# Performance work log

Hardware: AMD Instinct MI355X
Metric: run time of the kernel (lower is better)

## Reference

```python
import jax, jax.numpy as jnp
import numpy as np

D_MODEL = 2048
N_HEADS = 16
D_HEAD = D_MODEL // N_HEADS
BATCH = 2
SEQ = 2048
NEG = -1e9


def setup_inputs() -> dict:
    key = jax.random.key(0)
    ks = jax.random.split(key, 6)
    s = 1.0 / np.sqrt(D_MODEL)
    x = jax.random.normal(ks[0], (BATCH, SEQ, D_MODEL), dtype=jnp.float32)
    # additive causal mask: 0 on/below diagonal, -1e9 above
    causal = jnp.where(jnp.tril(jnp.ones((SEQ, SEQ), dtype=bool)), 0.0, NEG).astype(jnp.float32)
    return {
        "x": x,
        "mask": causal,
        "Wq": jax.random.normal(ks[1], (D_MODEL, D_MODEL), dtype=jnp.float32) * s,
        "bq": jnp.zeros((D_MODEL,), dtype=jnp.float32),
        "Wk": jax.random.normal(ks[2], (D_MODEL, D_MODEL), dtype=jnp.float32) * s,
        "bk": jnp.zeros((D_MODEL,), dtype=jnp.float32),
        "Wv": jax.random.normal(ks[3], (D_MODEL, D_MODEL), dtype=jnp.float32) * s,
        "bv": jnp.zeros((D_MODEL,), dtype=jnp.float32),
        "Wo": jax.random.normal(ks[4], (D_MODEL, D_MODEL), dtype=jnp.float32) * s,
        "bo": jnp.zeros((D_MODEL,), dtype=jnp.float32),
    }


def reference(x, mask, Wq, bq, Wk, bk, Wv, bv, Wo, bo):
    B, S, _ = x.shape
    scale = 1.0 / np.sqrt(D_HEAD).astype(np.float32)
    # projections -> (B, H, S, Dh)
    def split_heads(t):
        return t.reshape(B, S, N_HEADS, D_HEAD).transpose(0, 2, 1, 3)
    q = split_heads(x @ Wq + bq)
    k = split_heads(x @ Wk + bk)
    v = split_heads(x @ Wv + bv)
    scores = jnp.einsum("bhqd,bhkd->bhqk", q, k) * scale + mask  # (B,H,S,S)
    weights = jax.nn.softmax(scores, axis=-1)
    attn = jnp.einsum("bhqk,bhkd->bhqd", weights, v)
    attn = attn.transpose(0, 2, 1, 3).reshape(B, S, D_MODEL)
    return attn @ Wo + bo
```

## Files before the change

### kernel.cpp

```cpp
#include <hip/hip_runtime.h>
#include <hip/hip_bf16.h>
#include <math.h>

typedef __bf16 bf16;
typedef __attribute__((ext_vector_type(4))) __bf16 bf16x4;
typedef __attribute__((ext_vector_type(8))) __bf16 bf16x8;
typedef __attribute__((ext_vector_type(4))) float f32x4;
typedef __attribute__((ext_vector_type(4))) int i32x4;

#define DEV __device__ __forceinline__
#define FENCE asm volatile("" ::: "memory")

static constexpr int S_LEN = 2048;
static constexpr int DM = 2048;
static constexpr int NB = 2;
static constexpr int NH = 16;
static constexpr int DH = 128;
static constexpr long MROWS = (long)NB * S_LEN;

static constexpr float QSCALE = 0.12751744836522312f;
static constexpr float M0 = 11.0f;


__global__ void k_cast_bf16(const float* __restrict__ in, bf16* __restrict__ out, long n8) {
  long i = (long)blockIdx.x * blockDim.x + threadIdx.x;
  long stride = (long)gridDim.x * blockDim.x;
  for (; i < n8; i += stride) {
    const float4* p = (const float4*)(in + i * 8);
    float4 a = p[0], b = p[1];
    bf16x8 v;
    v[0] = (bf16)a.x; v[1] = (bf16)a.y; v[2] = (bf16)a.z; v[3] = (bf16)a.w;
    v[4] = (bf16)b.x; v[5] = (bf16)b.y; v[6] = (bf16)b.z; v[7] = (bf16)b.w;
    *(bf16x8*)(out + i * 8) = v;
  }
}

__global__ void k_transpose_w(const float* __restrict__ in, bf16* __restrict__ out) {
  __shared__ float t[32][33];
  int bx = blockIdx.x * 32, by = blockIdx.y * 32;
  int tx = threadIdx.x, ty = threadIdx.y;
#pragma unroll
  for (int i = 0; i < 32; i += 8)
    t[ty + i][tx] = in[(long)(by + ty + i) * DM + bx + tx];
  __syncthreads();
#pragma unroll
  for (int i = 0; i < 32; i += 8)
    out[(long)(bx + ty + i) * DM + by + tx] = (bf16)t[tx][ty + i];
}

__global__ void k_transpose_w3(const float* __restrict__ w0, const float* __restrict__ w1,
                               const float* __restrict__ w2, bf16* __restrict__ out) {
  __shared__ float t[32][33];
  int z = blockIdx.z;
  const float* in = (z == 0) ? w0 : (z == 1) ? w1 : w2;
  bf16* o = out + (long)z * DM * DM;
  int bx = blockIdx.x * 32, by = blockIdx.y * 32;
  int tx = threadIdx.x, ty = threadIdx.y;
#pragma unroll
  for (int i = 0; i < 32; i += 8)
    t[ty + i][tx] = in[(long)(by + ty + i) * DM + bx + tx];
  __syncthreads();
#pragma unroll
  for (int i = 0; i < 32; i += 8)
    o[(long)(bx + ty + i) * DM + by + tx] = (bf16)t[tx][ty + i];
}


DEV void stg_round(const bf16* __restrict__ g, long gstride, bf16* l, int tid, int c) {
  int o = c * 8192 + tid * 16;
  int row = o >> 7;
  int blk = (o >> 4) & 7;
  const bf16* src = g + (long)row * gstride + ((blk ^ (row & 7)) << 3);
  char* dst = (char*)l + (o & ~1023);
  __builtin_amdgcn_global_load_lds(
      (const __attribute__((address_space(1))) void*)src,
      (__attribute__((address_space(3))) void*)dst, 16, 0, 0);
}

template<int ROWB>
DEV void stage16k(const bf16* __restrict__ g, long gstride, bf16* l, int tid) {
#pragma unroll
  for (int c = 0; c < 4; ++c) {
    int o = c * 4096 + tid * 16;
    int row = o / ROWB;
    int blk = (o & (ROWB - 1)) >> 4;
    int blkg = blk ^ (row & 7);
    const bf16* src = g + (long)row * gstride + (blkg << 3);
    char* dst = (char*)l + (o & ~1023);
    __builtin_amdgcn_global_load_lds(
        (const __attribute__((address_space(1))) void*)src,
        (__attribute__((address_space(3))) void*)dst, 16, 0, 0);
  }
}

DEV void stage_k(const bf16* __restrict__ g, bf16* l, int tid) {
#pragma unroll
  for (int c = 0; c < 4; ++c) {
    int o = c * 4096 + tid * 16;
    int row = o >> 8;
    int blk = (o >> 4) & 15;
    int blkg = blk ^ (row & 7);
    int prow = (row & 3) | (((row >> 2) & 3) << 3) | (((row >> 5) & 1) << 2) |
               (((row >> 4) & 1) << 5);
    const bf16* src = g + (long)prow * DM + (blkg << 3);
    char* dst = (char*)l + (o & ~1023);
    __builtin_amdgcn_global_load_lds(
        (const __attribute__((address_space(1))) void*)src,
        (__attribute__((address_space(3))) void*)dst, 16, 0, 0);
  }
}

template<int ROWB>
DEV bf16x8 read_frag(const bf16* l, int row, int blk) {
  int blks = blk ^ (row & 7);
  return *(const bf16x8*)((const char*)l + row * ROWB + (blks << 4));
}


DEV void gemm_loop(const bf16* __restrict__ gA, const bf16* __restrict__ gB,
                   char* smem, int tid, int wm, int wn, int g, int c16,
                   f32x4 (&acc)[4][4]) {
#define BUFA(i) ((bf16*)(smem + (i) * 49152))
#define BUFB(i) ((bf16*)(smem + (i) * 49152 + 32768))

#pragma unroll
  for (int t0 = 0; t0 < 2; ++t0) {
#pragma unroll
    for (int c = 0; c < 4; ++c) stg_round(gA + t0 * 64, 2048, BUFA(t0), tid, c);
#pragma unroll
    for (int c = 0; c < 2; ++c) stg_round(gB + t0 * 64, 2048, BUFB(t0), tid, c);
  }
  asm volatile("s_waitcnt vmcnt(6)" ::: "memory");
  __builtin_amdgcn_s_barrier();
  FENCE;

#pragma unroll 1
  for (int t = 0; t < 32; ++t) {
    bf16* cA = BUFA(t % 3);
    bf16* cB = BUFB(t % 3);
    bf16* nA = BUFA((t + 2) % 3);
    bf16* nB = BUFB((t + 2) % 3);
    const bf16* gA2 = gA + (t + 2) * 64;
    const bf16* gB2 = gB + (t + 2) * 64;
    bool st = (t + 2) < 32;
    bf16x8 af[4], bj[4];

    if (st) { stg_round(gA2, 2048, nA, tid, 0); stg_round(gA2, 2048, nA, tid, 1);
              stg_round(gA2, 2048, nA, tid, 2); }
#pragma unroll
    for (int i = 0; i < 4; ++i) af[i] = read_frag<128>(cA, wm * 64 + i * 16 + c16, g);
#pragma unroll
    for (int j = 0; j < 4; ++j) bj[j] = read_frag<128>(cB, wn * 64 + j * 16 + c16, g);
    __builtin_amdgcn_s_setprio(1);
#pragma unroll
    for (int i = 0; i < 4; ++i)
#pragma unroll
      for (int j = 0; j < 4; ++j)
        acc[i][j] = __builtin_amdgcn_mfma_f32_16x16x32_bf16(af[i], bj[j], acc[i][j], 0, 0, 0);
    __builtin_amdgcn_s_setprio(0);
    FENCE; __builtin_amdgcn_s_barrier(); FENCE;

    if (st) { stg_round(gA2, 2048, nA, tid, 3);
              stg_round(gB2, 2048, nB, tid, 0); stg_round(gB2, 2048, nB, tid, 1); }
#pragma unroll
    for (int i = 0; i < 4; ++i) af[i] = read_frag<128>(cA, wm * 64 + i * 16 + c16, 4 + g);
#pragma unroll
    for (int j = 0; j < 4; ++j) bj[j] = read_frag<128>(cB, wn * 64 + j * 16 + c16, 4 + g);
    __builtin_amdgcn_s_setprio(1);
#pragma unroll
    for (int i = 0; i < 4; ++i)
#pragma unroll
      for (int j = 0; j < 4; ++j)
        acc[i][j] = __builtin_amdgcn_mfma_f32_16x16x32_bf16(af[i], bj[j], acc[i][j], 0, 0, 0);
    __builtin_amdgcn_s_setprio(0);
    if (t + 2 < 32) {
      asm volatile("s_waitcnt vmcnt(6)" ::: "memory");
    } else if (t + 1 < 32) {
      asm volatile("s_waitcnt vmcnt(0)" ::: "memory");
    }
    FENCE; __builtin_amdgcn_s_barrier(); FENCE;
  }
#undef BUFA
#undef BUFB
}

__global__ __launch_bounds__(512) void k_gemm_qkv(const bf16* __restrict__ A,
                                                  const bf16* __restrict__ WTqkv,
                                                  const float* __restrict__ bq,
                                                  const float* __restrict__ bk,
                                                  const float* __restrict__ bv,
                                                  bf16* __restrict__ Qb,
                                                  bf16* __restrict__ Kb,
                                                  bf16* __restrict__ Vt) {
  extern __shared__ char smem[];
  int tid = threadIdx.x;
  int w = tid >> 6, lane = tid & 63;
  int wm = w >> 1, wn = w & 1;
  int g = lane >> 4, c16 = lane & 15;
  long row0 = (long)blockIdx.y * 256;
  long col0 = (long)blockIdx.x * 128;
  int proj = (int)(col0 >> 11);
  int lcol0 = (int)(col0 & 2047);
  const float* bias = (proj == 0) ? bq : (proj == 1) ? bk : bv;

  f32x4 acc[4][4] = {};
  gemm_loop(A + row0 * 2048, WTqkv + col0 * 2048, smem, tid, wm, wn, g, c16, acc);

#pragma unroll
  for (int i = 0; i < 4; ++i) {
    long grow = row0 + wm * 64 + i * 16 + (g << 2);
#pragma unroll
    for (int j = 0; j < 4; ++j) {
      int lcol = lcol0 + wn * 64 + j * 16 + c16;
      float bv_ = bias[lcol];
      if (proj == 2) {
        int b = (int)(grow >> 11), s = (int)(grow & 2047);
        int h = lcol >> 7, d = lcol & 127;
        bf16x4 pk;
#pragma unroll
        for (int r = 0; r < 4; ++r) pk[r] = (bf16)(acc[i][j][r] + bv_);
        *(bf16x4*)(Vt + ((long)((b << 4) | h) * 128 + d) * 2048 + s) = pk;
      } else {
        bf16* dst = (proj == 0) ? Qb : Kb;
        float cs = (proj == 0) ? QSCALE : 1.0f;
#pragma unroll
        for (int r = 0; r < 4; ++r)
          dst[(grow + r) * 2048 + lcol] = (bf16)((acc[i][j][r] + bv_) * cs);
      }
    }
  }
}

__global__ __launch_bounds__(512) void k_gemm_o(const bf16* __restrict__ A,
                                                const bf16* __restrict__ BT,
                                                const float* __restrict__ bias,
                                                float* __restrict__ C) {
  extern __shared__ char smem[];
  int tid = threadIdx.x;
  int w = tid >> 6, lane = tid & 63;
  int wm = w >> 1, wn = w & 1;
  int g = lane >> 4, c16 = lane & 15;
  long row0 = (long)blockIdx.y * 256, col0 = (long)blockIdx.x * 128;

  f32x4 acc[4][4] = {};
  gemm_loop(A + row0 * 2048, BT + col0 * 2048, smem, tid, wm, wn, g, c16, acc);

#pragma unroll
  for (int i = 0; i < 4; ++i) {
    long grow = row0 + wm * 64 + i * 16 + (g << 2);
#pragma unroll
    for (int j = 0; j < 4; ++j) {
      long gcol = col0 + wn * 64 + j * 16 + c16;
      float bv = bias[gcol];
#pragma unroll
      for (int r = 0; r < 4; ++r)
        C[(grow + r) * 2048 + gcol] = acc[i][j][r] + bv;
    }
  }
}


__global__ __launch_bounds__(256, 2) void k_attn(const bf16* __restrict__ Q,
                                                 const bf16* __restrict__ Kt,
                                                 const bf16* __restrict__ Vt,
                                                 bf16* __restrict__ O,
                                                 bf16* __restrict__ part,
                                                 float* __restrict__ lsums) {
  __shared__ __align__(16) bf16 sK[2][64 * 128];
  __shared__ __align__(16) bf16 sV[2][128 * 64];

  int tid = threadIdx.x;
  int bid = blockIdx.x;
  int bh = bid & 31;
  int pr = (bid >> 5) & 7;
  int role = bid >> 8;
  int b = bh >> 4, h = bh & 15;
  int w = tid >> 6, lane = tid & 63;
  int g = lane >> 4, c16 = lane & 15;
  int t = bh * 8 + pr;

  const bf16* Qh = Q + (long)b * S_LEN * DM + h * DH;
  const bf16* Kh = Kt + (long)b * S_LEN * DM + h * DH;
  const bf16* Vh = Vt + (long)bh * DH * S_LEN;

#pragma unroll 1
  for (int seg = 0; seg < 2; ++seg) {
    int qt, k0, k1, partial;
    if (role == 0) {
      if (seg == 0) { qt = pr;      k0 = 0;           k1 = 2 * pr + 2;  partial = 0; }
      else          { qt = 15 - pr; k0 = 0;           k1 = 15 - 2 * pr; partial = 1; }
    } else {
      if (seg == 1) break;
      qt = 15 - pr; k0 = 15 - 2 * pr; k1 = 32 - 2 * pr; partial = 2;
    }

    int q0 = qt * 128;
    int qb = q0 + w * 32;

    bf16x8 qa[2][4];
#pragma unroll
    for (int u = 0; u < 2; ++u)
#pragma unroll
      for (int ks = 0; ks < 4; ++ks)
        qa[u][ks] = *(const bf16x8*)(Qh + (long)(qb + 16 * u + c16) * DM + (ks * 4 + g) * 8);

    stage_k(Kh + (long)k0 * 64 * DM, sK[0], tid);
    stage16k<128>(Vh + k0 * 64, S_LEN, sV[0], tid);

    float lsum[2] = {0.f, 0.f};
    f32x4 od[2][8] = {};

#pragma unroll 1
    for (int kt = k0; kt < k1; ++kt) {
      int cur = (kt - k0) & 1;
      if (kt + 1 < k1) {
        stage_k(Kh + (long)(kt + 1) * 64 * DM, sK[cur ^ 1], tid);
        stage16k<128>(Vh + (kt + 1) * 64, S_LEN, sV[cur ^ 1], tid);
        asm volatile("s_waitcnt vmcnt(8)" ::: "memory");
      } else {
        asm volatile("s_waitcnt vmcnt(0)" ::: "memory");
      }
      __builtin_amdgcn_s_barrier();
      FENCE;

      int kv0 = kt * 64;
      if (kv0 <= qb + 31) {
        f32x4 sf[2][4] = {};
        __builtin_amdgcn_s_setprio(1);
#pragma unroll
        for (int n = 0; n < 4; ++n)
#pragma unroll
          for (int ks = 0; ks < 4; ++ks) {
            bf16x8 kf = read_frag<256>(sK[cur], n * 16 + c16, ks * 4 + g);
            sf[0][n] = __builtin_amdgcn_mfma_f32_16x16x32_bf16(kf, qa[0][ks], sf[0][n], 0, 0, 0);
            sf[1][n] = __builtin_amdgcn_mfma_f32_16x16x32_bf16(kf, qa[1][ks], sf[1][n], 0, 0, 0);
          }
        __builtin_amdgcn_s_setprio(0);

        bool emask = (kv0 + 63 > qb);
        bf16x8 pa[2][2];
#pragma unroll
        for (int u = 0; u < 2; ++u) {
          unsigned pw[8];
#pragma unroll
          for (int n = 0; n < 4; ++n) {
            float pv4[4];
#pragma unroll
            for (int r = 0; r < 4; ++r) {
              float sc = sf[u][n][r];
              if (emask) {
                int kv = kv0 + ((n & 1) << 5) + (g << 3) + ((n >> 1) << 2) + r;
                int qg = qb + 16 * u + c16;
                sc = (kv > qg) ? -INFINITY : sc;
              }
              float pv = exp2f(sc - M0);
              pv4[r] = pv;
              lsum[u] += pv;
            }
            asm("v_cvt_pk_bf16_f32 %0, %1, %2" : "=v"(pw[2 * n]) : "v"(pv4[0]), "v"(pv4[1]));
            asm("v_cvt_pk_bf16_f32 %0, %1, %2" : "=v"(pw[2 * n + 1]) : "v"(pv4[2]), "v"(pv4[3]));
          }
          i32x4 t0 = {(int)pw[0], (int)pw[1], (int)pw[4], (int)pw[5]};
          i32x4 t1 = {(int)pw[2], (int)pw[3], (int)pw[6], (int)pw[7]};
          pa[u][0] = __builtin_bit_cast(bf16x8, t0);
          pa[u][1] = __builtin_bit_cast(bf16x8, t1);
        }

        __builtin_amdgcn_s_setprio(1);
#pragma unroll
        for (int j = 0; j < 8; ++j)
#pragma unroll
          for (int ks = 0; ks < 2; ++ks) {
            bf16x8 vf = read_frag<128>(sV[cur], j * 16 + c16, ks * 4 + g);
            od[0][j] = __builtin_amdgcn_mfma_f32_16x16x32_bf16(pa[0][ks], vf, od[0][j], 0, 0, 0);
            od[1][j] = __builtin_amdgcn_mfma_f32_16x16x32_bf16(pa[1][ks], vf, od[1][j], 0, 0, 0);
          }
        __builtin_amdgcn_s_setprio(0);
      }
      FENCE;
      __builtin_amdgcn_s_barrier();
    }

#pragma unroll
    for (int u = 0; u < 2; ++u) {
      lsum[u] += __shfl_xor(lsum[u], 16);
      lsum[u] += __shfl_xor(lsum[u], 32);
    }

    if (partial == 0) {
      const long ob = ((long)(b * S_LEN + qb)) * DM + h * DH + c16;
#pragma unroll
      for (int u = 0; u < 2; ++u)
#pragma unroll
        for (int r = 0; r < 4; ++r) {
          float inv = 1.0f / __shfl(lsum[u], 4 * g + r);
#pragma unroll
          for (int j = 0; j < 8; ++j)
            O[ob + (long)(16 * u + 4 * g + r) * DM + j * 16] = (bf16)(od[u][j][r] * inv);
        }
    } else {
      bf16* PP = part + ((long)((partial == 2 ? 256 : 0) + t)) * 16384;
      float* LP = lsums + (partial == 2 ? 256 * 128 : 0) + t * 128;
#pragma unroll
      for (int u = 0; u < 2; ++u) {
        if (g == 0) LP[32 * w + 16 * u + c16] = lsum[u];
#pragma unroll
        for (int r = 0; r < 4; ++r) {
          int row = 32 * w + 16 * u + 4 * g + r;
#pragma unroll
          for (int j = 0; j < 8; ++j)
            PP[row * 128 + 16 * j + c16] = (bf16)od[u][j][r];
        }
      }
    }
  }
}

__global__ __launch_bounds__(256) void k_merge(const bf16* __restrict__ part,
                                               const float* __restrict__ lsums,
                                               bf16* __restrict__ A2) {
  int t = blockIdx.x;
  int bh = t >> 3, pr = t & 7;
  int b = bh >> 4, h = bh & 15;
  int qt = 15 - pr;
  int tid = threadIdx.x;
  int q = tid >> 1, d0 = (tid & 1) * 64;
  float inv = 1.0f / (lsums[t * 128 + q] + lsums[256 * 128 + t * 128 + q]);
  const bf16* pA = part + (long)t * 16384 + q * 128 + d0;
  const bf16* pB = part + (long)(256 + t) * 16384 + q * 128 + d0;
  bf16* out = A2 + ((long)(b * S_LEN + qt * 128 + q)) * DM + h * DH + d0;
#pragma unroll
  for (int j = 0; j < 8; ++j) {
    bf16x8 a = *(const bf16x8*)(pA + j * 8);
    bf16x8 bb = *(const bf16x8*)(pB + j * 8);
    bf16x8 o;
#pragma unroll
    for (int r = 0; r < 8; ++r) o[r] = (bf16)(((float)a[r] + (float)bb[r]) * inv);
    *(bf16x8*)(out + j * 8) = o;
  }
}


extern "C" void kernel_launch(void* const* d_in, const int* in_sizes, int n_in,
                              void* d_out, int out_size, void* d_ws, size_t ws_size,
                              hipStream_t stream) {
  (void)in_sizes; (void)n_in; (void)out_size; (void)ws_size;
  const float* x  = (const float*)d_in[0];
  const float* Wq = (const float*)d_in[2];
  const float* bq = (const float*)d_in[3];
  const float* Wk = (const float*)d_in[4];
  const float* bk = (const float*)d_in[5];
  const float* Wv = (const float*)d_in[6];
  const float* bv = (const float*)d_in[7];
  const float* Wo = (const float*)d_in[8];
  const float* bo = (const float*)d_in[9];
  float* out = (float*)d_out;

  bf16* Xb = (bf16*)d_ws;
  bf16* WT = Xb + MROWS * DM;
  bf16* Qb = WT + (long)DM * DM;
  bf16* Kb = Qb + MROWS * DM;
  bf16* Vt = Kb + MROWS * DM;
  bf16* A2 = Xb;

  bf16* WTqkv = (bf16*)d_out;
  bf16* part = (bf16*)d_out;
  float* lsums = (float*)((bf16*)d_out + 2L * 256 * 16384);

  static const int GEMM_LDS = 3 * 49152;
  hipFuncSetAttribute((const void*)k_gemm_qkv, hipFuncAttributeMaxDynamicSharedMemorySize, GEMM_LDS);
  hipFuncSetAttribute((const void*)k_gemm_o, hipFuncAttributeMaxDynamicSharedMemorySize, GEMM_LDS);

  dim3 tb32(32, 8);
  dim3 gW(64, 64);

  k_cast_bf16<<<2048, 256, 0, stream>>>(x, Xb, MROWS * DM / 8);
  k_transpose_w3<<<dim3(64, 64, 3), tb32, 0, stream>>>(Wq, Wk, Wv, WTqkv);

  k_gemm_qkv<<<dim3(48, 16), 512, GEMM_LDS, stream>>>(Xb, WTqkv, bq, bk, bv, Qb, Kb, Vt);

  k_attn<<<512, 256, 0, stream>>>(Qb, Kb, Vt, A2, part, lsums);
  k_merge<<<256, 256, 0, stream>>>(part, lsums, A2);

  k_transpose_w<<<gW, tb32, 0, stream>>>(Wo, WT);
  k_gemm_o<<<dim3(16, 16), 512, GEMM_LDS, stream>>>(A2, WT, bo, out);
}
```

Measured before the change: 249.2 us.

## Widen QKV GEMM tile to 256x256 with double-buffered LDS pipeline

```diff
diff --git a/kernel.cpp b/kernel.cpp
--- a/kernel.cpp
+++ b/kernel.cpp
@@ -117,73 +117,6 @@
 }
 
 
-DEV void gemm_loop(const bf16* __restrict__ gA, const bf16* __restrict__ gB,
-                   char* smem, int tid, int wm, int wn, int g, int c16,
-                   f32x4 (&acc)[4][4]) {
-#define BUFA(i) ((bf16*)(smem + (i) * 49152))
-#define BUFB(i) ((bf16*)(smem + (i) * 49152 + 32768))
-
-#pragma unroll
-  for (int t0 = 0; t0 < 2; ++t0) {
-#pragma unroll
-    for (int c = 0; c < 4; ++c) stg_round(gA + t0 * 64, 2048, BUFA(t0), tid, c);
-#pragma unroll
-    for (int c = 0; c < 2; ++c) stg_round(gB + t0 * 64, 2048, BUFB(t0), tid, c);
-  }
-  asm volatile("s_waitcnt vmcnt(6)" ::: "memory");
-  __builtin_amdgcn_s_barrier();
-  FENCE;
-
-#pragma unroll 1
-  for (int t = 0; t < 32; ++t) {
-    bf16* cA = BUFA(t % 3);
-    bf16* cB = BUFB(t % 3);
-    bf16* nA = BUFA((t + 2) % 3);
-    bf16* nB = BUFB((t + 2) % 3);
-    const bf16* gA2 = gA + (t + 2) * 64;
-    const bf16* gB2 = gB + (t + 2) * 64;
-    bool st = (t + 2) < 32;
-    bf16x8 af[4], bj[4];
-
-    if (st) { stg_round(gA2, 2048, nA, tid, 0); stg_round(gA2, 2048, nA, tid, 1);
-              stg_round(gA2, 2048, nA, tid, 2); }
-#pragma unroll
-    for (int i = 0; i < 4; ++i) af[i] = read_frag<128>(cA, wm * 64 + i * 16 + c16, g);
-#pragma unroll
-    for (int j = 0; j < 4; ++j) bj[j] = read_frag<128>(cB, wn * 64 + j * 16 + c16, g);
-    __builtin_amdgcn_s_setprio(1);
-#pragma unroll
-    for (int i = 0; i < 4; ++i)
-#pragma unroll
-      for (int j = 0; j < 4; ++j)
-        acc[i][j] = __builtin_amdgcn_mfma_f32_16x16x32_bf16(af[i], bj[j], acc[i][j], 0, 0, 0);
-    __builtin_amdgcn_s_setprio(0);
-    FENCE; __builtin_amdgcn_s_barrier(); FENCE;
-
-    if (st) { stg_round(gA2, 2048, nA, tid, 3);
-              stg_round(gB2, 2048, nB, tid, 0); stg_round(gB2, 2048, nB, tid, 1); }
-#pragma unroll
-    for (int i = 0; i < 4; ++i) af[i] = read_frag<128>(cA, wm * 64 + i * 16 + c16, 4 + g);
-#pragma unroll
-    for (int j = 0; j < 4; ++j) bj[j] = read_frag<128>(cB, wn * 64 + j * 16 + c16, 4 + g);
-    __builtin_amdgcn_s_setprio(1);
-#pragma unroll
-    for (int i = 0; i < 4; ++i)
-#pragma unroll
-      for (int j = 0; j < 4; ++j)
-        acc[i][j] = __builtin_amdgcn_mfma_f32_16x16x32_bf16(af[i], bj[j], acc[i][j], 0, 0, 0);
-    __builtin_amdgcn_s_setprio(0);
-    if (t + 2 < 32) {
-      asm volatile("s_waitcnt vmcnt(6)" ::: "memory");
-    } else if (t + 1 < 32) {
-      asm volatile("s_waitcnt vmcnt(0)" ::: "memory");
-    }
-    FENCE; __builtin_amdgcn_s_barrier(); FENCE;
-  }
-#undef BUFA
-#undef BUFB
-}
-
 __global__ __launch_bounds__(512) void k_gemm_qkv(const bf16* __restrict__ A,
                                                   const bf16* __restrict__ WTqkv,
                                                   const float* __restrict__ bq,
@@ -195,20 +128,73 @@
   extern __shared__ char smem[];
   int tid = threadIdx.x;
   int w = tid >> 6, lane = tid & 63;
-  int wm = w >> 1, wn = w & 1;
+  int wm = w >> 2, wn = w & 3;
   int g = lane >> 4, c16 = lane & 15;
   long row0 = (long)blockIdx.y * 256;
-  long col0 = (long)blockIdx.x * 128;
+  long col0 = (long)blockIdx.x * 256;
   int proj = (int)(col0 >> 11);
   int lcol0 = (int)(col0 & 2047);
   const float* bias = (proj == 0) ? bq : (proj == 1) ? bk : bv;
-
-  f32x4 acc[4][4] = {};
-  gemm_loop(A + row0 * 2048, WTqkv + col0 * 2048, smem, tid, wm, wn, g, c16, acc);
-
-#pragma unroll
-  for (int i = 0; i < 4; ++i) {
-    long grow = row0 + wm * 64 + i * 16 + (g << 2);
+  const bf16* gA = A + row0 * 2048;
+  const bf16* gB = WTqkv + col0 * 2048;
+
+  f32x4 acc[8][4] = {};
+
+#define BA(i) ((bf16*)(smem + (i) * 65536))
+#define BB(i) ((bf16*)(smem + (i) * 65536 + 32768))
+
+#pragma unroll
+  for (int c = 0; c < 4; ++c) stg_round(gA, 2048, BA(0), tid, c);
+#pragma unroll
+  for (int c = 0; c < 4; ++c) stg_round(gB, 2048, BB(0), tid, c);
+  asm volatile("s_waitcnt vmcnt(0)" ::: "memory");
+  __builtin_amdgcn_s_barrier();
+  FENCE;
+
+#pragma unroll 1
+  for (int t = 0; t < 32; ++t) {
+    int cur = t & 1, nxt = cur ^ 1;
+    bf16* cA = BA(cur);
+    bf16* cB = BB(cur);
+    bool st = (t + 1) < 32;
+    if (st) {
+      const bf16* gA2 = gA + (t + 1) * 64;
+      const bf16* gB2 = gB + (t + 1) * 64;
+#pragma unroll
+      for (int c = 0; c < 4; ++c) stg_round(gA2, 2048, BA(nxt), tid, c);
+#pragma unroll
+      for (int c = 0; c < 4; ++c) stg_round(gB2, 2048, BB(nxt), tid, c);
+    }
+    bf16x8 af[4], bj[4];
+#pragma unroll
+    for (int ks = 0; ks < 2; ++ks) {
+#pragma unroll
+      for (int j = 0; j < 4; ++j)
+        bj[j] = read_frag<128>(cB, wn * 64 + j * 16 + c16, ks * 4 + g);
+#pragma unroll
+      for (int rh = 0; rh < 2; ++rh) {
+#pragma unroll
+        for (int i = 0; i < 4; ++i)
+          af[i] = read_frag<128>(cA, wm * 128 + rh * 64 + i * 16 + c16, ks * 4 + g);
+        __builtin_amdgcn_s_setprio(1);
+#pragma unroll
+        for (int i = 0; i < 4; ++i)
+#pragma unroll
+          for (int j = 0; j < 4; ++j)
+            acc[rh * 4 + i][j] =
+                __builtin_amdgcn_mfma_f32_16x16x32_bf16(af[i], bj[j], acc[rh * 4 + i][j], 0, 0, 0);
+        __builtin_amdgcn_s_setprio(0);
+      }
+    }
+    if (st) {
+      asm volatile("s_waitcnt vmcnt(0)" ::: "memory");
+      FENCE; __builtin_amdgcn_s_barrier(); FENCE;
+    }
+  }
+
+#pragma unroll
+  for (int i = 0; i < 8; ++i) {
+    long grow = row0 + wm * 128 + i * 16 + (g << 2);
 #pragma unroll
     for (int j = 0; j < 4; ++j) {
       int lcol = lcol0 + wn * 64 + j * 16 + c16;
@@ -229,6 +215,76 @@
       }
     }
   }
+#undef BA
+#undef BB
+}
+
+
+DEV void gemm_loop(const bf16* __restrict__ gA, const bf16* __restrict__ gB,
+                   char* smem, int tid, int wm, int wn, int g, int c16,
+                   f32x4 (&acc)[4][4]) {
+#define BUFA(i) ((bf16*)(smem + (i) * 49152))
+#define BUFB(i) ((bf16*)(smem + (i) * 49152 + 32768))
+
+#pragma unroll
+  for (int t0 = 0; t0 < 2; ++t0) {
+#pragma unroll
+    for (int c = 0; c < 4; ++c) stg_round(gA + t0 * 64, 2048, BUFA(t0), tid, c);
+#pragma unroll
+    for (int c = 0; c < 2; ++c) stg_round(gB + t0 * 64, 2048, BUFB(t0), tid, c);
+  }
+  asm volatile("s_waitcnt vmcnt(6)" ::: "memory");
+  __builtin_amdgcn_s_barrier();
+  FENCE;
+
+#pragma unroll 1
+  for (int t = 0; t < 32; ++t) {
+    bf16* cA = BUFA(t % 3);
+    bf16* cB = BUFB(t % 3);
+    bf16* nA = BUFA((t + 2) % 3);
+    bf16* nB = BUFB((t + 2) % 3);
+    const bf16* gA2 = gA + (t + 2) * 64;
+    const bf16* gB2 = gB + (t + 2) * 64;
+    bool st = (t + 2) < 32;
+    bf16x8 af[4], bj[4];
+
+    if (st) { stg_round(gA2, 2048, nA, tid, 0); stg_round(gA2, 2048, nA, tid, 1);
+              stg_round(gA2, 2048, nA, tid, 2); }
+#pragma unroll
+    for (int i = 0; i < 4; ++i) af[i] = read_frag<128>(cA, wm * 64 + i * 16 + c16, g);
+#pragma unroll
+    for (int j = 0; j < 4; ++j) bj[j] = read_frag<128>(cB, wn * 64 + j * 16 + c16, g);
+    __builtin_amdgcn_s_setprio(1);
+#pragma unroll
+    for (int i = 0; i < 4; ++i)
+#pragma unroll
+      for (int j = 0; j < 4; ++j)
+        acc[i][j] = __builtin_amdgcn_mfma_f32_16x16x32_bf16(af[i], bj[j], acc[i][j], 0, 0, 0);
+    __builtin_amdgcn_s_setprio(0);
+    FENCE; __builtin_amdgcn_s_barrier(); FENCE;
+
+    if (st) { stg_round(gA2, 2048, nA, tid, 3);
+              stg_round(gB2, 2048, nB, tid, 0); stg_round(gB2, 2048, nB, tid, 1); }
+#pragma unroll
+    for (int i = 0; i < 4; ++i) af[i] = read_frag<128>(cA, wm * 64 + i * 16 + c16, 4 + g);
+#pragma unroll
+    for (int j = 0; j < 4; ++j) bj[j] = read_frag<128>(cB, wn * 64 + j * 16 + c16, 4 + g);
+    __builtin_amdgcn_s_setprio(1);
+#pragma unroll
+    for (int i = 0; i < 4; ++i)
+#pragma unroll
+      for (int j = 0; j < 4; ++j)
+        acc[i][j] = __builtin_amdgcn_mfma_f32_16x16x32_bf16(af[i], bj[j], acc[i][j], 0, 0, 0);
+    __builtin_amdgcn_s_setprio(0);
+    if (t + 2 < 32) {
+      asm volatile("s_waitcnt vmcnt(6)" ::: "memory");
+    } else if (t + 1 < 32) {
+      asm volatile("s_waitcnt vmcnt(0)" ::: "memory");
+    }
+    FENCE; __builtin_amdgcn_s_barrier(); FENCE;
+  }
+#undef BUFA
+#undef BUFB
 }
 
 __global__ __launch_bounds__(512) void k_gemm_o(const bf16* __restrict__ A,
@@ -467,9 +523,10 @@
   bf16* part = (bf16*)d_out;
   float* lsums = (float*)((bf16*)d_out + 2L * 256 * 16384);
 
-  static const int GEMM_LDS = 3 * 49152;
-  hipFuncSetAttribute((const void*)k_gemm_qkv, hipFuncAttributeMaxDynamicSharedMemorySize, GEMM_LDS);
-  hipFuncSetAttribute((const void*)k_gemm_o, hipFuncAttributeMaxDynamicSharedMemorySize, GEMM_LDS);
+  static const int QKV_LDS = 2 * 65536;
+  static const int O_LDS = 3 * 49152;
+  hipFuncSetAttribute((const void*)k_gemm_qkv, hipFuncAttributeMaxDynamicSharedMemorySize, QKV_LDS);
+  hipFuncSetAttribute((const void*)k_gemm_o, hipFuncAttributeMaxDynamicSharedMemorySize, O_LDS);
 
   dim3 tb32(32, 8);
   dim3 gW(64, 64);
@@ -477,11 +534,11 @@
   k_cast_bf16<<<2048, 256, 0, stream>>>(x, Xb, MROWS * DM / 8);
   k_transpose_w3<<<dim3(64, 64, 3), tb32, 0, stream>>>(Wq, Wk, Wv, WTqkv);
 
-  k_gemm_qkv<<<dim3(48, 16), 512, GEMM_LDS, stream>>>(Xb, WTqkv, bq, bk, bv, Qb, Kb, Vt);
+  k_gemm_qkv<<<dim3(24, 16), 512, QKV_LDS, stream>>>(Xb, WTqkv, bq, bk, bv, Qb, Kb, Vt);
 
   k_attn<<<512, 256, 0, stream>>>(Qb, Kb, Vt, A2, part, lsums);
   k_merge<<<256, 256, 0, stream>>>(part, lsums, A2);
 
   k_transpose_w<<<gW, tb32, 0, stream>>>(Wo, WT);
-  k_gemm_o<<<dim3(16, 16), 512, GEMM_LDS, stream>>>(A2, WT, bo, out);
-}
+  k_gemm_o<<<dim3(16, 16), 512, O_LDS, stream>>>(A2, WT, bo, out);
+}
```

Result: slower. 254.8 us (+2.3%).

## Rebalance causal attention with table-driven split-K segments and single-buffered V

Applied to the files above, without the earlier changes.

```diff
diff --git a/kernel.cpp b/kernel.cpp
--- a/kernel.cpp
+++ b/kernel.cpp
@@ -260,24 +260,50 @@
 }
 
 
-__global__ __launch_bounds__(256, 2) void k_attn(const bf16* __restrict__ Q,
+__device__ const unsigned char SEGTAB[48][4] = {
+  {5,0,12,255},  {255,0,0,0},
+  {0,0,2,255},   {4,0,10,255},
+  {1,0,4,255},   {3,0,8,255},
+  {2,0,6,255},   {6,0,6,0},
+  {6,6,14,1},    {7,0,4,2},
+  {7,4,16,3},    {255,0,0,0},
+  {8,0,12,4},    {255,0,0,0},
+  {8,12,18,5},   {9,0,6,6},
+  {9,6,17,7},    {255,0,0,0},
+  {9,17,20,8},   {10,0,8,9},
+  {10,8,19,10},  {255,0,0,0},
+  {10,19,22,11}, {11,0,8,12},
+  {11,8,19,13},  {255,0,0,0},
+  {11,19,24,14}, {12,0,6,15},
+  {12,6,17,16},  {255,0,0,0},
+  {12,17,26,17}, {13,0,2,18},
+  {13,2,13,19},  {255,0,0,0},
+  {13,13,24,20}, {255,0,0,0},
+  {13,24,28,21}, {14,0,7,22},
+  {14,7,18,23},  {255,0,0,0},
+  {14,18,29,24}, {255,0,0,0},
+  {14,29,30,25}, {15,0,10,26},
+  {15,10,21,27}, {255,0,0,0},
+  {15,21,32,28}, {255,0,0,0}
+};
+__device__ const unsigned char MST[11] = {0,2,4,6,9,12,15,18,22,26,29};
+
+__global__ __launch_bounds__(256, 3) void k_attn(const bf16* __restrict__ Q,
                                                  const bf16* __restrict__ Kt,
                                                  const bf16* __restrict__ Vt,
                                                  bf16* __restrict__ O,
                                                  bf16* __restrict__ part,
                                                  float* __restrict__ lsums) {
   __shared__ __align__(16) bf16 sK[2][64 * 128];
-  __shared__ __align__(16) bf16 sV[2][128 * 64];
+  __shared__ __align__(16) bf16 sV[128 * 64];
 
   int tid = threadIdx.x;
   int bid = blockIdx.x;
   int bh = bid & 31;
-  int pr = (bid >> 5) & 7;
-  int role = bid >> 8;
+  int slot = bid >> 5;
   int b = bh >> 4, h = bh & 15;
   int w = tid >> 6, lane = tid & 63;
   int g = lane >> 4, c16 = lane & 15;
-  int t = bh * 8 + pr;
 
   const bf16* Qh = Q + (long)b * S_LEN * DM + h * DH;
   const bf16* Kh = Kt + (long)b * S_LEN * DM + h * DH;
@@ -285,17 +311,13 @@
 
 #pragma unroll 1
   for (int seg = 0; seg < 2; ++seg) {
-    int qt, k0, k1, partial;
-    if (role == 0) {
-      if (seg == 0) { qt = pr;      k0 = 0;           k1 = 2 * pr + 2;  partial = 0; }
-      else          { qt = 15 - pr; k0 = 0;           k1 = 15 - 2 * pr; partial = 1; }
-    } else {
-      if (seg == 1) break;
-      qt = 15 - pr; k0 = 15 - 2 * pr; k1 = 32 - 2 * pr; partial = 2;
-    }
-
-    int q0 = qt * 128;
-    int qb = q0 + w * 32;
+    int qt = SEGTAB[slot * 2 + seg][0];
+    if (qt == 255) break;
+    int k0 = SEGTAB[slot * 2 + seg][1];
+    int k1 = SEGTAB[slot * 2 + seg][2];
+    int pidx = SEGTAB[slot * 2 + seg][3];
+
+    int qb = qt * 128 + w * 32;
 
     bf16x8 qa[2][4];
 #pragma unroll
@@ -305,7 +327,6 @@
         qa[u][ks] = *(const bf16x8*)(Qh + (long)(qb + 16 * u + c16) * DM + (ks * 4 + g) * 8);
 
     stage_k(Kh + (long)k0 * 64 * DM, sK[0], tid);
-    stage16k<128>(Vh + k0 * 64, S_LEN, sV[0], tid);
 
     float lsum[2] = {0.f, 0.f};
     f32x4 od[2][8] = {};
@@ -313,65 +334,78 @@
 #pragma unroll 1
     for (int kt = k0; kt < k1; ++kt) {
       int cur = (kt - k0) & 1;
-      if (kt + 1 < k1) {
-        stage_k(Kh + (long)(kt + 1) * 64 * DM, sK[cur ^ 1], tid);
-        stage16k<128>(Vh + (kt + 1) * 64, S_LEN, sV[cur ^ 1], tid);
-        asm volatile("s_waitcnt vmcnt(8)" ::: "memory");
-      } else {
-        asm volatile("s_waitcnt vmcnt(0)" ::: "memory");
-      }
+      bool st = (kt + 1) < k1;
+      stage16k<128>(Vh + kt * 64, S_LEN, sV, tid);
+      if (st) stage_k(Kh + (long)(kt + 1) * 64 * DM, sK[cur ^ 1], tid);
+      if (st) asm volatile("s_waitcnt vmcnt(8)" ::: "memory");
+      else    asm volatile("s_waitcnt vmcnt(4)" ::: "memory");
       __builtin_amdgcn_s_barrier();
       FENCE;
 
       int kv0 = kt * 64;
-      if (kv0 <= qb + 31) {
-        f32x4 sf[2][4] = {};
-        __builtin_amdgcn_s_setprio(1);
-#pragma unroll
-        for (int n = 0; n < 4; ++n)
-#pragma unroll
-          for (int ks = 0; ks < 4; ++ks) {
-            bf16x8 kf = read_frag<256>(sK[cur], n * 16 + c16, ks * 4 + g);
-            sf[0][n] = __builtin_amdgcn_mfma_f32_16x16x32_bf16(kf, qa[0][ks], sf[0][n], 0, 0, 0);
-            sf[1][n] = __builtin_amdgcn_mfma_f32_16x16x32_bf16(kf, qa[1][ks], sf[1][n], 0, 0, 0);
+      bool active = (kv0 <= qb + 31);
+      bf16x8 pa[2][2];
+      if (active) {
+        bool emask = (kv0 + 63 > qb);
+        unsigned pw[2][8];
+#pragma unroll
+        for (int np = 0; np < 2; ++np) {
+          f32x4 sf[2][2] = {};
+          __builtin_amdgcn_s_setprio(1);
+#pragma unroll
+          for (int nn = 0; nn < 2; ++nn) {
+            int n = np * 2 + nn;
+#pragma unroll
+            for (int ks = 0; ks < 4; ++ks) {
+              bf16x8 kf = read_frag<256>(sK[cur], n * 16 + c16, ks * 4 + g);
+              sf[0][nn] = __builtin_amdgcn_mfma_f32_16x16x32_bf16(kf, qa[0][ks], sf[0][nn], 0, 0, 0);
+              sf[1][nn] = __builtin_amdgcn_mfma_f32_16x16x32_bf16(kf, qa[1][ks], sf[1][nn], 0, 0, 0);
+            }
           }
-        __builtin_amdgcn_s_setprio(0);
-
-        bool emask = (kv0 + 63 > qb);
-        bf16x8 pa[2][2];
+          __builtin_amdgcn_s_setprio(0);
+#pragma unroll
+          for (int u = 0; u < 2; ++u)
+#pragma unroll
+            for (int nn = 0; nn < 2; ++nn) {
+              int n = np * 2 + nn;
+              float pv4[4];
+#pragma unroll
+              for (int r = 0; r < 4; ++r) {
+                float sc = sf[u][nn][r];
+                if (emask) {
+                  int kv = kv0 + ((n & 1) << 5) + (g << 3) + ((n >> 1) << 2) + r;
+                  int qg = qb + 16 * u + c16;
+                  sc = (kv > qg) ? -INFINITY : sc;
+                }
+                float pv = exp2f(sc - M0);
+                pv4[r] = pv;
+                lsum[u] += pv;
+              }
+              asm("v_cvt_pk_bf16_f32 %0, %1, %2" : "=v"(pw[u][2 * n]) : "v"(pv4[0]), "v"(pv4[1]));
+              asm("v_cvt_pk_bf16_f32 %0, %1, %2" : "=v"(pw[u][2 * n + 1]) : "v"(pv4[2]), "v"(pv4[3]));
+            }
+        }
 #pragma unroll
         for (int u = 0; u < 2; ++u) {
-          unsigned pw[8];
-#pragma unroll
-          for (int n = 0; n < 4; ++n) {
-            float pv4[4];
-#pragma unroll
-            for (int r = 0; r < 4; ++r) {
-              float sc = sf[u][n][r];
-              if (emask) {
-                int kv = kv0 + ((n & 1) << 5) + (g << 3) + ((n >> 1) << 2) + r;
-                int qg = qb + 16 * u + c16;
-                sc = (kv > qg) ? -INFINITY : sc;
-              }
-              float pv = exp2f(sc - M0);
-              pv4[r] = pv;
-              lsum[u] += pv;
-            }
-            asm("v_cvt_pk_bf16_f32 %0, %1, %2" : "=v"(pw[2 * n]) : "v"(pv4[0]), "v"(pv4[1]));
-            asm("v_cvt_pk_bf16_f32 %0, %1, %2" : "=v"(pw[2 * n + 1]) : "v"(pv4[2]), "v"(pv4[3]));
-          }
-          i32x4 t0 = {(int)pw[0], (int)pw[1], (int)pw[4], (int)pw[5]};
-          i32x4 t1 = {(int)pw[2], (int)pw[3], (int)pw[6], (int)pw[7]};
+          i32x4 t0 = {(int)pw[u][0], (int)pw[u][1], (int)pw[u][4], (int)pw[u][5]};
+          i32x4 t1 = {(int)pw[u][2], (int)pw[u][3], (int)pw[u][6], (int)pw[u][7]};
           pa[u][0] = __builtin_bit_cast(bf16x8, t0);
           pa[u][1] = __builtin_bit_cast(bf16x8, t1);
         }
-
+      }
+
+      if (st) asm volatile("s_waitcnt vmcnt(4)" ::: "memory");
+      else    asm volatile("s_waitcnt vmcnt(0)" ::: "memory");
+      __builtin_amdgcn_s_barrier();
+      FENCE;
+
+      if (active) {
         __builtin_amdgcn_s_setprio(1);
 #pragma unroll
         for (int j = 0; j < 8; ++j)
 #pragma unroll
           for (int ks = 0; ks < 2; ++ks) {
-            bf16x8 vf = read_frag<128>(sV[cur], j * 16 + c16, ks * 4 + g);
+            bf16x8 vf = read_frag<128>(sV, j * 16 + c16, ks * 4 + g);
             od[0][j] = __builtin_amdgcn_mfma_f32_16x16x32_bf16(pa[0][ks], vf, od[0][j], 0, 0, 0);
             od[1][j] = __builtin_amdgcn_mfma_f32_16x16x32_bf16(pa[1][ks], vf, od[1][j], 0, 0, 0);
           }
@@ -387,7 +421,7 @@
       lsum[u] += __shfl_xor(lsum[u], 32);
     }
 
-    if (partial == 0) {
+    if (pidx == 255) {
       const long ob = ((long)(b * S_LEN + qb)) * DM + h * DH + c16;
 #pragma unroll
       for (int u = 0; u < 2; ++u)
@@ -399,8 +433,8 @@
             O[ob + (long)(16 * u + 4 * g + r) * DM + j * 16] = (bf16)(od[u][j][r] * inv);
         }
     } else {
-      bf16* PP = part + ((long)((partial == 2 ? 256 : 0) + t)) * 16384;
-      float* LP = lsums + (partial == 2 ? 256 * 128 : 0) + t * 128;
+      bf16* PP = part + (long)(bh * 32 + pidx) * 16384;
+      float* LP = lsums + (bh * 32 + pidx) * 128;
 #pragma unroll
       for (int u = 0; u < 2; ++u) {
         if (g == 0) LP[32 * w + 16 * u + c16] = lsum[u];
@@ -420,22 +454,27 @@
                                                const float* __restrict__ lsums,
                                                bf16* __restrict__ A2) {
   int t = blockIdx.x;
-  int bh = t >> 3, pr = t & 7;
+  int bh = t / 10, sj = t % 10;
+  int qt = 6 + sj;
   int b = bh >> 4, h = bh & 15;
-  int qt = 15 - pr;
   int tid = threadIdx.x;
   int q = tid >> 1, d0 = (tid & 1) * 64;
-  float inv = 1.0f / (lsums[t * 128 + q] + lsums[256 * 128 + t * 128 + q]);
-  const bf16* pA = part + (long)t * 16384 + q * 128 + d0;
-  const bf16* pB = part + (long)(256 + t) * 16384 + q * 128 + d0;
+  int p0 = MST[sj], p1 = MST[sj + 1];
+  float ls = 0.f;
+  for (int p = p0; p < p1; ++p) ls += lsums[(bh * 32 + p) * 128 + q];
+  float inv = 1.0f / ls;
   bf16* out = A2 + ((long)(b * S_LEN + qt * 128 + q)) * DM + h * DH + d0;
 #pragma unroll
   for (int j = 0; j < 8; ++j) {
-    bf16x8 a = *(const bf16x8*)(pA + j * 8);
-    bf16x8 bb = *(const bf16x8*)(pB + j * 8);
+    float acc[8] = {};
+    for (int p = p0; p < p1; ++p) {
+      bf16x8 v = *(const bf16x8*)(part + (long)(bh * 32 + p) * 16384 + q * 128 + d0 + j * 8);
+#pragma unroll
+      for (int r = 0; r < 8; ++r) acc[r] += (float)v[r];
+    }
     bf16x8 o;
 #pragma unroll
-    for (int r = 0; r < 8; ++r) o[r] = (bf16)(((float)a[r] + (float)bb[r]) * inv);
+    for (int r = 0; r < 8; ++r) o[r] = (bf16)(acc[r] * inv);
     *(bf16x8*)(out + j * 8) = o;
   }
 }
@@ -465,7 +504,7 @@
 
   bf16* WTqkv = (bf16*)d_out;
   bf16* part = (bf16*)d_out;
-  float* lsums = (float*)((bf16*)d_out + 2L * 256 * 16384);
+  float* lsums = (float*)WT;
 
   static const int GEMM_LDS = 3 * 49152;
   hipFuncSetAttribute((const void*)k_gemm_qkv, hipFuncAttributeMaxDynamicSharedMemorySize, GEMM_LDS);
@@ -479,8 +518,8 @@
 
   k_gemm_qkv<<<dim3(48, 16), 512, GEMM_LDS, stream>>>(Xb, WTqkv, bq, bk, bv, Qb, Kb, Vt);
 
-  k_attn<<<512, 256, 0, stream>>>(Qb, Kb, Vt, A2, part, lsums);
-  k_merge<<<256, 256, 0, stream>>>(part, lsums, A2);
+  k_attn<<<768, 256, 0, stream>>>(Qb, Kb, Vt, A2, part, lsums);
+  k_merge<<<320, 256, 0, stream>>>(part, lsums, A2);
 
   k_transpose_w<<<gW, tb32, 0, stream>>>(Wo, WT);
   k_gemm_o<<<dim3(16, 16), 512, GEMM_LDS, stream>>>(A2, WT, bo, out);
```

After: 315.3 us. 26.5% more time.
